# Performance work log

Hardware: AMD Instinct MI355X
Metric: run time of the kernel (lower is better)

The kernel has to match this reference:

```python
import jax, jax.numpy as jnp
import numpy as np

B, S, D, H = 8, 2048, 1024, 8
CHUNK = D // H
SCALE = float(D) ** (-0.5)  # key_dim ** -0.5, key_dim == num_units here
LN_EPS = 1e-5


def setup_inputs() -> dict:
    key = jax.random.key(0)
    ks = jax.random.split(key, 9)
    s = 0.02
    return {
        "query": jax.random.normal(ks[0], (B, S, D), jnp.float32),
        "keys": jax.random.normal(ks[1], (B, S, D), jnp.float32),
        "Wq": jax.random.normal(ks[2], (D, D), jnp.float32) * s,  # torch Linear weight [out,in]
        "Wk": jax.random.normal(ks[3], (D, D), jnp.float32) * s,
        "Wv": jax.random.normal(ks[4], (D, D), jnp.float32) * s,
        "Wp": jax.random.normal(ks[5], (D, D), jnp.float32) * s,
        "bp": jnp.zeros((D,), jnp.float32),
        "ln_gamma": jnp.ones((D,), jnp.float32),
        "ln_beta": jnp.zeros((D,), jnp.float32),
    }


def reference(query, keys, Wq, Wk, Wv, Wp, bp, ln_gamma, ln_beta):
    # Linear layers (no bias on q/k/v): y = x @ W.T
    Q = jnp.einsum("bsd,ed->bse", query, Wq)
    K = jnp.einsum("bsd,ed->bse", keys, Wk)
    V = jnp.einsum("bsd,ed->bse", keys, Wv)
    # Faithful to original: raw view to [B*h, S, chunk] (no transpose head split)
    Qh = Q.reshape(B * H, S, CHUNK)
    Kh = K.reshape(B * H, S, CHUNK)
    Vh = V.reshape(B * H, S, CHUNK)
    # scores [B*h, S, S], scale, softmax (is_masked=False, dropout_p=0)
    att = jnp.einsum("gqc,gkc->gqk", Qh, Kh) * SCALE
    att = jax.nn.softmax(att, axis=-1)
    ctx = jnp.einsum("gqk,gkc->gqc", att, Vh).reshape(B, S, D)
    # output projection + residual + LayerNorm
    out = jnp.einsum("bsd,ed->bse", ctx, Wp) + bp
    out = out + query
    mu = jnp.mean(out, axis=-1, keepdims=True)
    var = jnp.mean(jnp.square(out - mu), axis=-1, keepdims=True)
    out = (out - mu) * jax.lax.rsqrt(var + LN_EPS) * ln_gamma + ln_beta
    return out
```

## Files before the change

kernel.cpp:

```cpp
#include <hip/hip_runtime.h>

typedef __bf16 bf16x8 __attribute__((ext_vector_type(8)));
typedef float f32x4 __attribute__((ext_vector_type(4)));
typedef float f32x16 __attribute__((ext_vector_type(16)));
typedef unsigned uint2e __attribute__((ext_vector_type(2)));

#define SCLOG 0.04508422f

__device__ __forceinline__ unsigned short f2bf(float f) {
  union { float f; unsigned int u; } v;
  v.f = f;
  unsigned int u = v.u;
  u += 0x7fffu + ((u >> 16) & 1u);
  return (unsigned short)(u >> 16);
}

__device__ __forceinline__ void gld_lds16(const void* g, void* l) {
  __builtin_amdgcn_global_load_lds(
      (const __attribute__((address_space(1))) void*)g,
      (__attribute__((address_space(3))) void*)l, 16, 0, 0);
}

__global__ __launch_bounds__(256) void convert_kernel(
    const float* __restrict__ q, const float* __restrict__ k,
    const float* __restrict__ wq, const float* __restrict__ wk,
    const float* __restrict__ wv, const float* __restrict__ wp,
    unsigned short* __restrict__ qb, unsigned short* __restrict__ kb,
    unsigned short* __restrict__ Wqkv, unsigned short* __restrict__ Wpb) {
  size_t i = (size_t)blockIdx.x * 256 + threadIdx.x;
  const float* src; unsigned short* dst; size_t off;
  if (i < 4194304)      { src = q;  dst = qb;             off = i; }
  else if (i < 8388608) { src = k;  dst = kb;             off = i - 4194304; }
  else if (i < 8650752) { src = wq; dst = Wqkv;           off = i - 8388608; }
  else if (i < 8912896) { src = wk; dst = Wqkv + 1048576; off = i - 8650752; }
  else if (i < 9175040) { src = wv; dst = Wqkv + 2097152; off = i - 8912896; }
  else                  { src = wp; dst = Wpb;            off = i - 9175040; }
  float4 v = ((const float4*)src)[off];
  ushort4 o;
  o.x = f2bf(v.x); o.y = f2bf(v.y); o.z = f2bf(v.z); o.w = f2bf(v.w);
  ((ushort4*)dst)[off] = o;
}

#define QKV_BAR __builtin_amdgcn_s_barrier()
#define QKV_LGKM asm volatile("s_waitcnt lgkmcnt(0)" ::: "memory")

#define QKV_STG(lc, h, srcb, s)                                               \
  gld_lds16((srcb) + (size_t)(s) * 128 + gro0, (lc) + (h) * 16384 + d0);      \
  gld_lds16((srcb) + (size_t)(s) * 128 + gro1, (lc) + (h) * 16384 + d0 + 1024);

#define QKV_RDA(I0)                                                           \
  _Pragma("unroll") for (int i4 = 0; i4 < 4; ++i4) {                          \
    af[i4][0] = *(const bf16x8*)(tb + rbA + ((I0) + i4) * 2048 + cx0);        \
    af[i4][1] = *(const bf16x8*)(tb + rbA + ((I0) + i4) * 2048 + cx1);        \
  }

#define QKV_RDB(JP)                                                           \
  _Pragma("unroll") for (int j2 = 0; j2 < 2; ++j2) {                          \
    bfr[JP][j2][0] = *(const bf16x8*)(tb + rbB + ((JP) * 2 + j2) * 2048 + cx0); \
    bfr[JP][j2][1] = *(const bf16x8*)(tb + rbB + ((JP) * 2 + j2) * 2048 + cx1); \
  }

#define QKV_MM(I0, JP)                                                        \
  _Pragma("unroll") for (int i4 = 0; i4 < 4; ++i4)                            \
  _Pragma("unroll") for (int j2 = 0; j2 < 2; ++j2)                            \
  _Pragma("unroll") for (int kk = 0; kk < 2; ++kk)                            \
    acc[(I0) + i4][(JP) * 2 + j2] = __builtin_amdgcn_mfma_f32_16x16x32_bf16(  \
        af[i4][kk], bfr[JP][j2][kk], acc[(I0) + i4][(JP) * 2 + j2], 0, 0, 0);

#define QKV_KLOOP                                                             \
  _Pragma("unroll")                                                           \
  for (int s = 0; s < 2; ++s) {                                               \
    char* lc = lds + s * 65536;                                               \
    QKV_STG(lc, 0, aBase, s);                                                 \
    QKV_STG(lc, 1, aBase + 262144, s);                                        \
    QKV_STG(lc + 32768, 0, bBase, s);                                         \
    QKV_STG(lc + 32768, 1, bBase + 262144, s);                                \
  }                                                                           \
  asm volatile("s_waitcnt vmcnt(8)" ::: "memory");                            \
  QKV_BAR;                                                                    \
  _Pragma("unroll 1")                                                         \
  for (int kt = 0; kt < 16; ++kt) {                                           \
    const char* tb = lds + (kt & 1) * 65536;                                  \
    char* lc = lds + (kt & 1) * 65536;                                        \
    const int s = kt + 2;                                                     \
    bf16x8 af[4][2], bfr[2][2][2];                                            \
    QKV_RDA(0);                                                               \
    QKV_RDB(0);                                                               \
    QKV_BAR; QKV_LGKM;                                                        \
    __builtin_amdgcn_s_setprio(1);                                            \
    QKV_MM(0, 0);                                                             \
    __builtin_amdgcn_s_setprio(0);                                            \
    QKV_BAR;                                                                  \
    QKV_RDB(1);                                                               \
    QKV_BAR; QKV_LGKM;                                                        \
    __builtin_amdgcn_s_setprio(1);                                            \
    QKV_MM(0, 1);                                                             \
    __builtin_amdgcn_s_setprio(0);                                            \
    QKV_BAR;                                                                  \
    QKV_RDA(4);                                                               \
    if (s < 16) {                                                             \
      QKV_STG(lc + 32768, 0, bBase, s);                                       \
      QKV_STG(lc + 32768, 1, bBase + 262144, s);                              \
    }                                                                         \
    QKV_BAR; QKV_LGKM;                                                        \
    __builtin_amdgcn_s_setprio(1);                                            \
    QKV_MM(4, 1);                                                             \
    __builtin_amdgcn_s_setprio(0);                                            \
    QKV_BAR;                                                                  \
    if (s < 16) {                                                             \
      QKV_STG(lc, 0, aBase, s);                                               \
      QKV_STG(lc, 1, aBase + 262144, s);                                      \
    }                                                                         \
    QKV_BAR;                                                                  \
    __builtin_amdgcn_s_setprio(1);                                            \
    QKV_MM(4, 0);                                                             \
    __builtin_amdgcn_s_setprio(0);                                            \
    if (kt <= 13)      { asm volatile("s_waitcnt vmcnt(8)" ::: "memory"); }   \
    else if (kt == 14) { asm volatile("s_waitcnt vmcnt(0)" ::: "memory"); }   \
    if (kt < 15) QKV_BAR;                                                     \
  }

#define QKV_COMMON_DECLS                                                      \
  const int t = threadIdx.x;                                                  \
  const int lane = t & 63;                                                    \
  const int w = t >> 6;                                                       \
  const int fr = lane & 15;                                                   \
  const int quad = lane >> 4;                                                 \
  const int wm2 = w >> 2, wn4 = w & 3;                                        \
  const size_t gro0 = (size_t)(w * 16 + (lane >> 3)) * 2048 +                 \
                      (size_t)(((lane & 7) ^ (lane >> 3)) << 4);              \
  const size_t gro1 = gro0 + 8 * 2048;                                        \
  const int d0 = w * 2048 + lane * 16;                                        \
  const int rbA = (wm2 * 128 + fr) * 128;                                     \
  const int rbB = 32768 + (wn4 * 64 + fr) * 128;                              \
  const int cx0 = (quad * 16) ^ ((fr & 7) << 4);                              \
  const int cx1 = cx0 ^ 64;

__global__ __launch_bounds__(512, 2) void gemm_qkv8_kernel(
    const unsigned short* __restrict__ qb,
    const unsigned short* __restrict__ kb,
    const unsigned short* __restrict__ W,
    unsigned short* __restrict__ Qo,
    unsigned short* __restrict__ Ko,
    unsigned short* __restrict__ Vo) {
  __shared__ char lds[131072];
  QKV_COMMON_DECLS

  const int orig = blockIdx.x;
  const int sseq = orig >> 3;
  const int tn = sseq >> 3;
  const int tm = (orig & 7) * 8 + (sseq & 7);

  const unsigned short* Ap = (tn < 4) ? qb : kb;
  const char* aBase = (const char*)Ap + (size_t)(tm * 256) * 2048;
  const char* bBase = (const char*)W + (size_t)(tn * 256) * 2048;

  f32x4 acc[8][4];
#pragma unroll
  for (int i = 0; i < 8; ++i)
#pragma unroll
    for (int j = 0; j < 4; ++j) acc[i][j] = (f32x4){0.f, 0.f, 0.f, 0.f};

  QKV_KLOOP

  const int sel = tn >> 2;
  unsigned short* Out = sel == 0 ? Qo : (sel == 1 ? Ko : Vo);
  const float osc = (sel == 0) ? SCLOG : 1.f;
  const int row0 = tm * 256 + wm2 * 128 + quad * 4;
  const int col0 = (tn & 3) * 256 + wn4 * 64 + fr;
#pragma unroll
  for (int i = 0; i < 8; ++i)
#pragma unroll
    for (int j = 0; j < 4; ++j)
#pragma unroll
      for (int r = 0; r < 4; ++r)
        Out[(size_t)(row0 + i * 16 + r) * 1024 + col0 + j * 16] = f2bf(acc[i][j][r] * osc);
}

__global__ __launch_bounds__(512, 2) void gemm_proj8_kernel(
    const unsigned short* __restrict__ A,
    const unsigned short* __restrict__ W,
    const float* __restrict__ bp,
    const float* __restrict__ qres,
    float* __restrict__ out) {
  __shared__ char lds[131072];
  QKV_COMMON_DECLS

  const int orig = blockIdx.x;
  const int sseq = orig >> 3;
  const int tn = sseq >> 3;
  const int tm = (orig & 7) * 8 + (sseq & 7);

  const char* aBase = (const char*)A + (size_t)(tm * 256) * 2048;
  const char* bBase = (const char*)W + (size_t)(tn * 256) * 2048;

  f32x4 acc[8][4];
#pragma unroll
  for (int i = 0; i < 8; ++i)
#pragma unroll
    for (int j = 0; j < 4; ++j) acc[i][j] = (f32x4){0.f, 0.f, 0.f, 0.f};

  QKV_KLOOP

  const int row0 = tm * 256 + wm2 * 128 + quad * 4;
  const int col0 = tn * 256 + wn4 * 64 + fr;
#pragma unroll
  for (int i = 0; i < 8; ++i)
#pragma unroll
    for (int j = 0; j < 4; ++j) {
      const int col = col0 + j * 16;
      const float bpc = bp[col];
#pragma unroll
      for (int r = 0; r < 4; ++r) {
        const size_t idx = (size_t)(row0 + i * 16 + r) * 1024 + col;
        out[idx] = acc[i][j][r] + bpc + qres[idx];
      }
    }
}

__global__ __launch_bounds__(256) void vtrans_kernel(
    const unsigned short* __restrict__ V, unsigned short* __restrict__ Vt) {
  __shared__ unsigned short T[128 * 136];
  const int g  = blockIdx.x >> 4;
  const int kt = blockIdx.x & 15;
  const unsigned short* Vg = V + (size_t)g * 262144 + (size_t)kt * 128 * 128;
  unsigned short* Vtg = Vt + (size_t)g * 262144 + kt * 128;
  const int t = threadIdx.x;
#pragma unroll
  for (int it = 0; it < 8; it++) {
    int seg = t + it * 256;
    int k  = seg >> 4;
    int c8 = (seg & 15) << 3;
    uint4 a = *(const uint4*)(Vg + k * 128 + c8);
    unsigned short* Tp = &T[c8 * 136 + k];
    Tp[0 * 136] = (unsigned short)(a.x & 0xffff);
    Tp[1 * 136] = (unsigned short)(a.x >> 16);
    Tp[2 * 136] = (unsigned short)(a.y & 0xffff);
    Tp[3 * 136] = (unsigned short)(a.y >> 16);
    Tp[4 * 136] = (unsigned short)(a.z & 0xffff);
    Tp[5 * 136] = (unsigned short)(a.z >> 16);
    Tp[6 * 136] = (unsigned short)(a.w & 0xffff);
    Tp[7 * 136] = (unsigned short)(a.w >> 16);
  }
  __syncthreads();
#pragma unroll
  for (int it = 0; it < 8; it++) {
    int seg = t + it * 256;
    int c  = seg >> 4;
    int k8 = (seg & 15) << 3;
    uint4 o = *(const uint4*)&T[c * 136 + k8];
    *(uint4*)(Vtg + (size_t)c * 2048 + k8) = o;
  }
}

#define PACK_HALF(EX, KSBASE)                                                  \
    _Pragma("unroll")                                                          \
    for (int c2 = 0; c2 < 2; c2++)                                             \
      _Pragma("unroll")                                                        \
      for (int e = 0; e < 2; e++) {                                            \
        unsigned ua, ub;                                                       \
        asm("v_cvt_pk_bf16_f32 %0, %1, %2" : "=v"(ua)                          \
            : "v"(EX[8 * c2 + 2 * e]), "v"(EX[8 * c2 + 2 * e + 1]));           \
        asm("v_cvt_pk_bf16_f32 %0, %1, %2" : "=v"(ub)                          \
            : "v"(EX[8 * c2 + 4 + 2 * e]), "v"(EX[8 * c2 + 4 + 2 * e + 1]));   \
        uint2e rr = __builtin_amdgcn_permlane32_swap(ua, ub, false, false);    \
        if (e == 0) { paw[(KSBASE) + c2].x = rr[0]; paw[(KSBASE) + c2].z = rr[1]; } \
        else        { paw[(KSBASE) + c2].y = rr[0]; paw[(KSBASE) + c2].w = rr[1]; } \
      }

#define ATTN_TILE(KSH, VSH, KST, VST, PREF)                                    \
  {                                                                            \
    if (PREF) {                                                                \
      gld_lds16(kp + kS0, (KST) + kD0);                                        \
      gld_lds16(kp + kS1, (KST) + kD1);                                        \
      gld_lds16(vp + vS0, (VST) + vD0);                                        \
      gld_lds16(vp + vS1, (VST) + vD1);                                        \
      kp += 8192; vp += 64;                                                    \
    }                                                                          \
    f32x16 s0, s1;                                                             \
    _Pragma("unroll")                                                          \
    for (int r = 0; r < 16; r++) { s0[r] = 0.f; s1[r] = 0.f; }                 \
    {                                                                          \
      bf16x8 kf[8];                                                            \
      _Pragma("unroll")                                                        \
      for (int ks = 0; ks < 8; ks++)                                           \
        kf[ks] = *(const bf16x8*)((KSH) + kb0 + kOf[ks]);                      \
      _Pragma("unroll")                                                        \
      for (int ks = 0; ks < 8; ks++)                                           \
        s0 = __builtin_amdgcn_mfma_f32_32x32x16_bf16(kf[ks], qf[ks], s0, 0, 0, 0); \
    }                                                                          \
    {                                                                          \
      bf16x8 kf[8];                                                            \
      _Pragma("unroll")                                                        \
      for (int ks = 0; ks < 8; ks++)                                           \
        kf[ks] = *(const bf16x8*)((KSH) + kb0 + 8192 + kOf[ks]);               \
      _Pragma("unroll")                                                        \
      for (int ks = 0; ks < 8; ks++)                                           \
        s1 = __builtin_amdgcn_mfma_f32_32x32x16_bf16(kf[ks], qf[ks], s1, 0, 0, 0); \
    }                                                                          \
    float ex0[16], ex1[16];                                                    \
    _Pragma("unroll")                                                          \
    for (int r = 0; r < 16; r++) {                                             \
      ex0[r] = __builtin_amdgcn_exp2f(fminf(s0[r], 30.f));                     \
      ex1[r] = __builtin_amdgcn_exp2f(fminf(s1[r], 30.f));                     \
      lp += ex0[r] + ex1[r];                                                   \
    }                                                                          \
    uint4 paw[4];                                                              \
    PACK_HALF(ex0, 0)                                                          \
    PACK_HALF(ex1, 2)                                                          \
    _Pragma("unroll")                                                          \
    for (int cb = 0; cb < 4; cb++) {                                           \
      _Pragma("unroll")                                                        \
      for (int ks = 0; ks < 4; ks++) {                                         \
        bf16x8 vf = *(const bf16x8*)((VSH) + cb * 4096 + vOf[ks]);             \
        bf16x8 pa8 = __builtin_bit_cast(bf16x8, paw[ks]);                      \
        O[cb] = __builtin_amdgcn_mfma_f32_32x32x16_bf16(pa8, vf, O[cb], 0, 0, 0); \
      }                                                                        \
    }                                                                          \
    __syncthreads();                                                           \
  }

__global__ __launch_bounds__(512, 1) void attn_kernel(
    const unsigned short* __restrict__ Q,
    const unsigned short* __restrict__ K,
    const unsigned short* __restrict__ Vt,
    unsigned short* __restrict__ ctx) {
  __shared__ unsigned char smem[65536];

  const int bid = blockIdx.x;
  const int g  = (bid & 7) * 8 + (bid >> 6);
  const int qt = (bid >> 3) & 7;
  const unsigned short* Qg = Q + (size_t)g * 262144 + (size_t)qt * 32768;
  const unsigned short* Kg = K + (size_t)g * 262144;
  const unsigned short* Vg = Vt + (size_t)g * 262144;

  const int t    = threadIdx.x;
  const int lane = t & 63;
  const int wv   = t >> 6;
  const int col  = lane & 31;
  const int hi   = lane >> 5;
  const int qrow = wv * 32 + col;

  int kOf[8];
#pragma unroll
  for (int ks = 0; ks < 8; ks++) {
    int c = ks * 2 + hi;
    kOf[ks] = (c ^ (col & 15)) << 4;
  }
  const int kb0 = col * 256;
  int vOf[4];
#pragma unroll
  for (int ks = 0; ks < 4; ks++) {
    int c = ks * 2 + hi;
    vOf[ks] = col * 128 + (((c ^ (col & 7) ^ ((col >> 3) & 1)) & 7) << 4);
  }
  int kS0, kS1, kD0, kD1, vS0, vS1, vD0, vD1;
  {
    int seg0 = t, seg1 = t + 512;
    int r0 = seg0 >> 4, p0 = seg0 & 15;
    int r1 = seg1 >> 4, p1 = seg1 & 15;
    kS0 = r0 * 128 + (p0 ^ (r0 & 15)) * 8;  kD0 = seg0 * 16;
    kS1 = r1 * 128 + (p1 ^ (r1 & 15)) * 8;  kD1 = seg1 * 16;
    int vr0 = seg0 >> 3, vp0 = seg0 & 7;
    int vr1 = seg1 >> 3, vp1 = seg1 & 7;
    vS0 = vr0 * 2048 + ((vp0 ^ (vr0 & 7) ^ ((vr0 >> 3) & 1)) & 7) * 8;  vD0 = seg0 * 16;
    vS1 = vr1 * 2048 + ((vp1 ^ (vr1 & 7) ^ ((vr1 >> 3) & 1)) & 7) * 8;  vD1 = seg1 * 16;
  }

#pragma unroll
  for (int it = 0; it < 8; it++) {
    int seg = t + it * 512;
    int r = seg >> 4, p = seg & 15;
    int c = p ^ (r & 15);
    gld_lds16(Qg + r * 128 + c * 8, smem + seg * 16);
  }
  __syncthreads();
  bf16x8 qf[8];
#pragma unroll
  for (int ks = 0; ks < 8; ks++) {
    int c = ks * 2 + hi;
    int p = c ^ (qrow & 15);
    qf[ks] = *(const bf16x8*)(smem + qrow * 256 + p * 16);
  }
  __syncthreads();

  gld_lds16(Kg + kS0, smem + kD0);
  gld_lds16(Kg + kS1, smem + kD1);
  gld_lds16(Vg + vS0, smem + 32768 + vD0);
  gld_lds16(Vg + vS1, smem + 32768 + vD1);
  __syncthreads();

  const unsigned short* kp = Kg + 8192;
  const unsigned short* vp = Vg + 64;

  f32x16 O[4];
#pragma unroll
  for (int cb = 0; cb < 4; cb++)
#pragma unroll
    for (int r = 0; r < 16; r++) O[cb][r] = 0.f;
  float lp = 0.f;

  unsigned char* B0K = smem;
  unsigned char* B1K = smem + 16384;
  unsigned char* B0V = smem + 32768;
  unsigned char* B1V = smem + 49152;

#pragma unroll 1
  for (int kt2 = 0; kt2 < 16; kt2++) {
    ATTN_TILE(B0K, B0V, B1K, B1V, 1);
    ATTN_TILE(B1K, B1V, B0K, B0V, (kt2 < 15));
  }

  lp += __shfl_xor(lp, 32);
  float* linv_arr = (float*)smem;
  linv_arr[wv * 32 + col] = 1.f / lp;
  float4 li[4];
#pragma unroll
  for (int rq = 0; rq < 4; rq++)
    li[rq] = *(const float4*)&linv_arr[wv * 32 + rq * 8 + hi * 4];

  unsigned short* Cg = ctx + (size_t)g * 262144 + (size_t)qt * 32768;
#pragma unroll
  for (int cb = 0; cb < 4; cb++)
#pragma unroll
    for (int rq = 0; rq < 4; rq++)
#pragma unroll
      for (int j = 0; j < 4; j++) {
        int row = wv * 32 + rq * 8 + hi * 4 + j;
        Cg[(size_t)row * 128 + cb * 32 + col] = f2bf(O[cb][rq * 4 + j] * li[rq][j]);
      }
}

__global__ __launch_bounds__(256) void ln_kernel(float* __restrict__ out,
                                                 const float* __restrict__ gamma,
                                                 const float* __restrict__ beta) {
  __shared__ float red[8];
  const int row = blockIdx.x;
  float* p = out + (size_t)row * 1024;
  const int t = threadIdx.x;
  float4 v = ((const float4*)p)[t];
  float s  = v.x + v.y + v.z + v.w;
  float s2 = v.x * v.x + v.y * v.y + v.z * v.z + v.w * v.w;
#pragma unroll
  for (int off = 1; off < 64; off <<= 1) {
    s  += __shfl_xor(s, off);
    s2 += __shfl_xor(s2, off);
  }
  const int wv = t >> 6;
  if ((t & 63) == 0) { red[wv] = s; red[4 + wv] = s2; }
  __syncthreads();
  float S  = red[0] + red[1] + red[2] + red[3];
  float S2 = red[4] + red[5] + red[6] + red[7];
  float mu  = S * (1.f / 1024.f);
  float var = S2 * (1.f / 1024.f) - mu * mu;
  float rstd = rsqrtf(var + 1e-5f);
  float4 gm = ((const float4*)gamma)[t];
  float4 bt = ((const float4*)beta)[t];
  v.x = (v.x - mu) * rstd * gm.x + bt.x;
  v.y = (v.y - mu) * rstd * gm.y + bt.y;
  v.z = (v.z - mu) * rstd * gm.z + bt.z;
  v.w = (v.w - mu) * rstd * gm.w + bt.w;
  ((float4*)p)[t] = v;
}

extern "C" void kernel_launch(void* const* d_in, const int* in_sizes, int n_in,
                              void* d_out, int out_size, void* d_ws, size_t ws_size,
                              hipStream_t stream) {
  const float* query = (const float*)d_in[0];
  const float* keys  = (const float*)d_in[1];
  const float* Wq    = (const float*)d_in[2];
  const float* Wk    = (const float*)d_in[3];
  const float* Wv    = (const float*)d_in[4];
  const float* Wp    = (const float*)d_in[5];
  const float* bp    = (const float*)d_in[6];
  const float* gamma = (const float*)d_in[7];
  const float* beta  = (const float*)d_in[8];
  float* out = (float*)d_out;

  unsigned short* ws   = (unsigned short*)d_ws;
  unsigned short* qb   = ws;
  unsigned short* kb   = ws + 16777216;
  unsigned short* Wqkv = ws + 33554432;
  unsigned short* Wpb  = ws + 36700160;
  unsigned short* Qb   = ws + 37748736;
  unsigned short* Kb   = ws + 54525952;
  unsigned short* Vb   = ws + 71303168;
  unsigned short* Vtb  = kb;
  unsigned short* ctx  = qb;

  convert_kernel<<<36864, 256, 0, stream>>>(query, keys, Wq, Wk, Wv, Wp, qb, kb, Wqkv, Wpb);
  gemm_qkv8_kernel<<<768, 512, 0, stream>>>(qb, kb, Wqkv, Qb, Kb, Vb);
  vtrans_kernel<<<1024, 256, 0, stream>>>(Vb, Vtb);
  attn_kernel<<<512, 512, 0, stream>>>(Qb, Kb, Vtb, ctx);
  gemm_proj8_kernel<<<256, 512, 0, stream>>>(ctx, Wpb, bp, query, out);
  ln_kernel<<<16384, 256, 0, stream>>>(out, gamma, beta);
}
```

Before: 507.1 us.

## Fuse V transpose into QKV GEMM epilogue and add setprio around attention MFMAs

The QKV GEMM now writes the V output directly in the transposed per-head layout, and the separate vtrans kernel is dropped. This saves a launch and a full read/write pass over V. The transposed stores are scattered 2-byte writes, which may coalesce poorly. The attention tile also raises wave priority during its MFMA sections, to improve overlap with the other waves' softmax work.

Result: slower. 578.5 us (+14.1%).

```diff
diff --git a/kernel.cpp b/kernel.cpp
--- a/kernel.cpp
+++ b/kernel.cpp
@@ -142,7 +142,7 @@
     const unsigned short* __restrict__ W,
     unsigned short* __restrict__ Qo,
     unsigned short* __restrict__ Ko,
-    unsigned short* __restrict__ Vo) {
+    unsigned short* __restrict__ Vt) {
   __shared__ char lds[131072];
   QKV_COMMON_DECLS
 
@@ -164,17 +164,36 @@
   QKV_KLOOP
 
   const int sel = tn >> 2;
-  unsigned short* Out = sel == 0 ? Qo : (sel == 1 ? Ko : Vo);
-  const float osc = (sel == 0) ? SCLOG : 1.f;
-  const int row0 = tm * 256 + wm2 * 128 + quad * 4;
-  const int col0 = (tn & 3) * 256 + wn4 * 64 + fr;
-#pragma unroll
-  for (int i = 0; i < 8; ++i)
-#pragma unroll
-    for (int j = 0; j < 4; ++j)
-#pragma unroll
-      for (int r = 0; r < 4; ++r)
-        Out[(size_t)(row0 + i * 16 + r) * 1024 + col0 + j * 16] = f2bf(acc[i][j][r] * osc);
+  if (sel < 2) {
+    unsigned short* Out = sel == 0 ? Qo : Ko;
+    const float osc = (sel == 0) ? SCLOG : 1.f;
+    const int row0 = tm * 256 + wm2 * 128 + quad * 4;
+    const int col0 = (tn & 3) * 256 + wn4 * 64 + fr;
+#pragma unroll
+    for (int i = 0; i < 8; ++i)
+#pragma unroll
+      for (int j = 0; j < 4; ++j)
+#pragma unroll
+        for (int r = 0; r < 4; ++r)
+          Out[(size_t)(row0 + i * 16 + r) * 1024 + col0 + j * 16] = f2bf(acc[i][j][r] * osc);
+  } else {
+    unsigned short* Vtg = Vt + (size_t)tm * 262144;
+    const int rowB = wm2 * 128 + quad * 4;
+    const int colL0 = wn4 * 64 + fr;
+    const int tnb = (tn & 3) * 2;
+#pragma unroll
+    for (int i = 0; i < 8; ++i)
+#pragma unroll
+      for (int j = 0; j < 4; ++j) {
+        const int colL = colL0 + j * 16;
+        const size_t cbase = (size_t)(colL & 127) * 2048 + tnb + (colL >> 7);
+#pragma unroll
+        for (int r = 0; r < 4; ++r) {
+          const int rowIn = rowB + i * 16 + r;
+          Vtg[cbase + rowIn * 8] = f2bf(acc[i][j][r]);
+        }
+      }
+  }
 }
 
 __global__ __launch_bounds__(512, 2) void gemm_proj8_kernel(
@@ -216,41 +235,6 @@
         out[idx] = acc[i][j][r] + bpc + qres[idx];
       }
     }
-}
-
-__global__ __launch_bounds__(256) void vtrans_kernel(
-    const unsigned short* __restrict__ V, unsigned short* __restrict__ Vt) {
-  __shared__ unsigned short T[128 * 136];
-  const int g  = blockIdx.x >> 4;
-  const int kt = blockIdx.x & 15;
-  const unsigned short* Vg = V + (size_t)g * 262144 + (size_t)kt * 128 * 128;
-  unsigned short* Vtg = Vt + (size_t)g * 262144 + kt * 128;
-  const int t = threadIdx.x;
-#pragma unroll
-  for (int it = 0; it < 8; it++) {
-    int seg = t + it * 256;
-    int k  = seg >> 4;
-    int c8 = (seg & 15) << 3;
-    uint4 a = *(const uint4*)(Vg + k * 128 + c8);
-    unsigned short* Tp = &T[c8 * 136 + k];
-    Tp[0 * 136] = (unsigned short)(a.x & 0xffff);
-    Tp[1 * 136] = (unsigned short)(a.x >> 16);
-    Tp[2 * 136] = (unsigned short)(a.y & 0xffff);
-    Tp[3 * 136] = (unsigned short)(a.y >> 16);
-    Tp[4 * 136] = (unsigned short)(a.z & 0xffff);
-    Tp[5 * 136] = (unsigned short)(a.z >> 16);
-    Tp[6 * 136] = (unsigned short)(a.w & 0xffff);
-    Tp[7 * 136] = (unsigned short)(a.w >> 16);
-  }
-  __syncthreads();
-#pragma unroll
-  for (int it = 0; it < 8; it++) {
-    int seg = t + it * 256;
-    int c  = seg >> 4;
-    int k8 = (seg & 15) << 3;
-    uint4 o = *(const uint4*)&T[c * 136 + k8];
-    *(uint4*)(Vtg + (size_t)c * 2048 + k8) = o;
-  }
 }
 
 #define PACK_HALF(EX, KSBASE)                                                  \
@@ -280,6 +264,7 @@
     f32x16 s0, s1;                                                             \
     _Pragma("unroll")                                                          \
     for (int r = 0; r < 16; r++) { s0[r] = 0.f; s1[r] = 0.f; }                 \
+    __builtin_amdgcn_s_setprio(1);                                             \
     {                                                                          \
       bf16x8 kf[8];                                                            \
       _Pragma("unroll")                                                        \
@@ -298,6 +283,7 @@
       for (int ks = 0; ks < 8; ks++)                                           \
         s1 = __builtin_amdgcn_mfma_f32_32x32x16_bf16(kf[ks], qf[ks], s1, 0, 0, 0); \
     }                                                                          \
+    __builtin_amdgcn_s_setprio(0);                                             \
     float ex0[16], ex1[16];                                                    \
     _Pragma("unroll")                                                          \
     for (int r = 0; r < 16; r++) {                                             \
@@ -308,6 +294,7 @@
     uint4 paw[4];                                                              \
     PACK_HALF(ex0, 0)                                                          \
     PACK_HALF(ex1, 2)                                                          \
+    __builtin_amdgcn_s_setprio(1);                                             \
     _Pragma("unroll")                                                          \
     for (int cb = 0; cb < 4; cb++) {                                           \
       _Pragma("unroll")                                                        \
@@ -317,6 +304,7 @@
         O[cb] = __builtin_amdgcn_mfma_f32_32x32x16_bf16(pa8, vf, O[cb], 0, 0, 0); \
       }                                                                        \
     }                                                                          \
+    __builtin_amdgcn_s_setprio(0);                                             \
     __syncthreads();                                                           \
   }
 
@@ -484,13 +472,11 @@
   unsigned short* Wpb  = ws + 36700160;
   unsigned short* Qb   = ws + 37748736;
   unsigned short* Kb   = ws + 54525952;
-  unsigned short* Vb   = ws + 71303168;
-  unsigned short* Vtb  = kb;
+  unsigned short* Vtb  = ws + 71303168;
   unsigned short* ctx  = qb;
 
   convert_kernel<<<36864, 256, 0, stream>>>(query, keys, Wq, Wk, Wv, Wp, qb, kb, Wqkv, Wpb);
-  gemm_qkv8_kernel<<<768, 512, 0, stream>>>(qb, kb, Wqkv, Qb, Kb, Vb);
-  vtrans_kernel<<<1024, 256, 0, stream>>>(Vb, Vtb);
+  gemm_qkv8_kernel<<<768, 512, 0, stream>>>(qb, kb, Wqkv, Qb, Kb, Vtb);
   attn_kernel<<<512, 512, 0, stream>>>(Qb, Kb, Vtb, ctx);
   gemm_proj8_kernel<<<256, 512, 0, stream>>>(ctx, Wpb, bp, query, out);
   ln_kernel<<<16384, 256, 0, stream>>>(out, gamma, beta);
```
